# Kernel optimization log

Measured on AMD Instinct MI355X. Metric: run time of the kernel, lower is better.

Reference implementation:

```python
import jax, jax.numpy as jnp
import numpy as np

# ---- static config (LCNN wirenet) ----
K = 128            # fixed junction count per type (n_dyn_junc // n_type)
N_PTS0 = 32
N_PTS1 = 8
SCALE = N_PTS0 // N_PTS1   # maxpool1d kernel/stride = 4
DIM_LOI = 128
DIM_FC = 1024
FEATURE_DIM = 8
USE_COOD = 0.0
USE_SLOP = 0.0
HW = 128
B = 2
# static u<v pair indices (torch: meshgrid -> c = u < v), P = K*(K-1)/2
IU_np, IV_np = np.triu_indices(K, k=1)
P = IU_np.shape[0]
IU = jnp.asarray(IU_np, jnp.int32)
IV = jnp.asarray(IV_np, jnp.int32)
LAMBDA = jnp.linspace(0.0, 1.0, N_PTS0)[:, None]  # [32,1]


def setup_inputs() -> dict:
    key = jax.random.key(0)
    ks = jax.random.split(key, 8)
    inputs = jax.random.normal(ks[0], (B, 5, HW, HW), jnp.float32)
    features = jax.random.normal(ks[1], (B, 256, HW, HW), jnp.float32)
    fc1_w = jax.random.normal(ks[2], (DIM_LOI, 256), jnp.float32) * 0.05
    fc1_b = jnp.zeros((DIM_LOI,), jnp.float32)
    d_in = DIM_LOI * N_PTS1 + FEATURE_DIM  # 1032
    w1 = jax.random.normal(ks[3], (d_in, DIM_FC), jnp.float32) * 0.03
    b1 = jnp.zeros((DIM_FC,), jnp.float32)
    w2 = jax.random.normal(ks[4], (DIM_FC, DIM_FC), jnp.float32) * 0.03
    b2 = jnp.zeros((DIM_FC,), jnp.float32)
    w3 = jax.random.normal(ks[5], (DIM_FC, 1), jnp.float32) * 0.03
    b3 = jnp.zeros((1,), jnp.float32)
    return dict(inputs=inputs, features=features, fc1_w=fc1_w, fc1_b=fc1_b,
                w1=w1, b1=b1, w2=w2, b2=b2, w3=w3, b3=b3)


def _nms(a):
    # a: [1,H,W]; 3x3 max-pool NMS, keep only local maxima
    ap = jax.lax.reduce_window(a, -jnp.inf, jax.lax.max, (1, 3, 3), (1, 1, 1), 'SAME')
    return a * (a == ap).astype(a.dtype)


def _sample_lines(jmap, joff):
    # jmap: [1,H,W], joff: [1,2,H,W]  (inference path: dummy junc/Lpos)
    n_type = 1
    jm = _nms(jmap).reshape(n_type, -1)            # [1, HW*HW]
    jo = joff.reshape(n_type, 2, -1)
    score, index = jax.lax.top_k(jm, K)            # [1,K]
    y = (index // HW).astype(jnp.float32) + jnp.take_along_axis(jo[:, 0], index, 1) + 0.5
    x = (index % HW).astype(jnp.float32) + jnp.take_along_axis(jo[:, 1], index, 1) + 0.5
    xy = jnp.stack([y, x], -1)                     # [1,K,2]
    # inference dummies: junc=zeros(1,2), jtyp=zeros(1), Lpos=zeros(2,2)
    junc = jnp.zeros((1, 2), jnp.float32)
    jtyp = jnp.zeros((1,), jnp.int32)
    dist = jnp.sum((xy[:, :, None, :] - junc) ** 2, -1)  # [1,K,1]
    cost = jnp.min(dist, -1)
    match = jnp.argmin(dist, -1).astype(jnp.int32)       # [1,K]
    Njunc = 1
    match = jnp.where(jtyp[match] != jnp.arange(n_type, dtype=jnp.int32)[:, None], Njunc, match)
    match = jnp.where(cost > 1.5 * 1.5, Njunc, match).reshape(-1)  # [K]
    up, vp = match[IU], match[IV]
    Lpos = jnp.zeros((2, 2), jnp.float32)
    label = Lpos[up, vp]                           # [P]
    xyf = xy.reshape(n_type * K, 2)
    xyu, xyv = xyf[IU], xyf[IV]                    # [P,2]
    u2v = xyu - xyv
    u2v = u2v / jnp.clip(jnp.sqrt(jnp.sum(u2v ** 2, -1, keepdims=True)), 1e-6)
    feat = jnp.concatenate([
        xyu / HW * USE_COOD, xyv / HW * USE_COOD, u2v * USE_SLOP,
        (IU[:, None] > K).astype(jnp.float32), (IV[:, None] > K).astype(jnp.float32)], 1)  # [P,8]
    line = jnp.stack([xyu, xyv], 1)                # [P,2,2]
    return line, label, feat


def _loi_pool(xfeat, line):
    # xfeat: [C,H,W], line: [P,2,2] -> [P,C,N_PTS1]
    p = line[:, 0:1, :] * LAMBDA + line[:, 1:2, :] * (1.0 - LAMBDA) - 0.5  # [P,32,2]
    p = p.reshape(-1, 2)
    px, py = p[:, 0], p[:, 1]
    px0 = jnp.clip(jnp.floor(px), 0, HW - 1)
    py0 = jnp.clip(jnp.floor(py), 0, HW - 1)
    px1 = jnp.clip(px0 + 1, 0, HW - 1)
    py1 = jnp.clip(py0 + 1, 0, HW - 1)
    px0l = px0.astype(jnp.int32); py0l = py0.astype(jnp.int32)
    px1l = px1.astype(jnp.int32); py1l = py1.astype(jnp.int32)
    xp = (xfeat[:, px0l, py0l] * (px1 - px) * (py1 - py)
          + xfeat[:, px1l, py0l] * (px - px0) * (py1 - py)
          + xfeat[:, px0l, py1l] * (px1 - px) * (py - py0)
          + xfeat[:, px1l, py1l] * (px - px0) * (py - py0))  # [C, P*32]
    xp = xp.reshape(DIM_LOI, -1, N_PTS0).transpose(1, 0, 2)  # [P,C,32]
    # MaxPool1d(kernel=4, stride=4)
    return xp.reshape(xp.shape[0], DIM_LOI, N_PTS1, SCALE).max(-1)  # [P,C,8]


def _forward(inputs, features, fc1_w, fc1_b, w1, b1, w2, b2, w3, b3):
    b, _, r, c = inputs.shape
    out = jnp.transpose(inputs, (1, 0, 2, 3))       # [5,B,H,W]
    jmap_logits = out[0:2].reshape(1, 2, b, r, c)
    joff_logits = out[3:5].reshape(1, 2, b, r, c)
    jmap = jax.nn.softmax(jnp.transpose(jmap_logits, (2, 0, 1, 3, 4)), axis=2)[:, :, 1]  # [B,1,H,W]
    joff = jax.nn.sigmoid(jnp.transpose(joff_logits, (2, 0, 1, 3, 4))) - 0.5             # [B,1,2,H,W]
    # fc1: 1x1 conv 256 -> dim_loi
    xf = jnp.einsum('bchw,dc->bdhw', features, fc1_w) + fc1_b[None, :, None, None]
    lines, labels, feats = jax.vmap(_sample_lines)(jmap, joff)   # [B,P,2,2],[B,P],[B,P,8]
    # sample_lines runs under torch.no_grad()
    lines = jax.lax.stop_gradient(lines)
    labels = jax.lax.stop_gradient(labels)
    feats = jax.lax.stop_gradient(feats)
    xp = jax.vmap(_loi_pool)(xf, lines)             # [B,P,C,8]
    xv = xp.reshape(-1, N_PTS1 * DIM_LOI)           # [B*P, 1024] (C-major then pts)
    xv = jnp.concatenate([xv, feats.reshape(-1, FEATURE_DIM)], 1)  # [B*P, 1032]
    h = jax.nn.relu(xv @ w1 + b1)
    h = jax.nn.relu(h @ w2 + b2)
    scores = (h @ w3 + b3).reshape(-1)              # [B*P]
    return scores, labels.reshape(-1), lines


def reference(inputs, features, fc1_w, fc1_b, w1, b1, w2, b2, w3, b3):
    return _forward(inputs, features, fc1_w, fc1_b, w1, b1, w2, b2, w3, b3)
```

## Files before the change

### kernel.cpp

```cpp
#include <hip/hip_runtime.h>
#include <hip/hip_bf16.h>
#include <math.h>

#define HW 128
#define NPIX 16384
#define KTOP 128
#define PPAIR 8128
#define NB 2
#define DIMLOI 128
#define NROWS (NB*PPAIR)
#define MPAD 16384

typedef __bf16 bf16x8 __attribute__((ext_vector_type(8)));
typedef float floatx4 __attribute__((ext_vector_type(4)));
typedef float floatx8 __attribute__((ext_vector_type(8)));

__device__ __forceinline__ unsigned long long mk_key(float v, int idx) {
    return ((unsigned long long)__float_as_uint(v) << 32) |
           (unsigned long long)(0xFFFFFFFFu - (unsigned)idx);
}

__device__ __forceinline__ unsigned long long shfl_xor_u64(unsigned long long x, int m) {
    unsigned lo = (unsigned)x, hi = (unsigned)(x >> 32);
    lo = __shfl_xor(lo, m);
    hi = __shfl_xor(hi, m);
    return ((unsigned long long)hi << 32) | lo;
}

__device__ __forceinline__ void bitonic_stage(unsigned long long V[4], int lane, int j, int k) {
    if (j >= 64) {
        int qm = j >> 6;
        #pragma unroll
        for (int q = 0; q < 4; q++) {
            int p = q ^ qm;
            if (p > q) {
                int i = q * 64 + lane;
                bool desc = ((i & k) == 0);
                unsigned long long a = V[q], b = V[p];
                unsigned long long hi = a > b ? a : b, lo = a > b ? b : a;
                V[q] = desc ? hi : lo;
                V[p] = desc ? lo : hi;
            }
        }
    } else {
        #pragma unroll
        for (int q = 0; q < 4; q++) {
            int i = q * 64 + lane;
            unsigned long long p = shfl_xor_u64(V[q], j);
            bool lower = (lane & j) == 0;
            bool desc = ((i & k) == 0);
            bool keepmax = (desc == lower);
            unsigned long long mx = V[q] > p ? V[q] : p;
            unsigned long long mn = V[q] > p ? p : V[q];
            V[q] = keepmax ? mx : mn;
        }
    }
}

__device__ __forceinline__ void sort256_desc(unsigned long long V[4], int lane) {
    #pragma unroll
    for (int k = 2; k <= 256; k <<= 1)
        #pragma unroll
        for (int j = k >> 1; j >= 1; j >>= 1)
            bitonic_stage(V, lane, j, k);
}

__device__ __forceinline__ void merge256_desc(unsigned long long V[4], int lane) {
    #pragma unroll
    for (int j = 128; j >= 1; j >>= 1)
        bitonic_stage(V, lane, j, 256);
}

__global__ __launch_bounds__(256) void nms_sort_kernel(const float* __restrict__ inp,
                                                       unsigned long long* __restrict__ tkeys) {
    __shared__ float jm[10 * HW];
    __shared__ unsigned long long cand[256];
    __shared__ int scnt;
    int blk = blockIdx.x;
    int b   = blockIdx.y;
    int tid = threadIdx.x, lane = tid & 63;
    int r0  = blk * 8;
    int rlo = (r0 > 0) ? r0 - 1 : 0;
    int rhi = (r0 + 8 < HW) ? r0 + 8 : HW - 1;
    int nrows = rhi - rlo + 1;

    for (int i = tid; i < nrows * HW; i += 256) {
        int pix = rlo * HW + i;
        float l0 = inp[((long)b * 5 + 0) * NPIX + pix];
        float l1 = inp[((long)b * 5 + 1) * NPIX + pix];
        float m = fmaxf(l0, l1);
        float e0 = expf(l0 - m), e1 = expf(l1 - m);
        jm[i] = e1 / (e0 + e1);
    }
    cand[tid] = 0ull;
    if (tid == 0) scnt = 0;
    __syncthreads();

    #pragma unroll
    for (int i = 0; i < 4; i++) {
        int pl = i * 256 + tid;
        int r = r0 + (pl >> 7), c = pl & 127;
        float v = jm[(r - rlo) * HW + c];
        float m = v;
        for (int dr = -1; dr <= 1; dr++) {
            int rr = r + dr;
            if (rr < 0 || rr >= HW) continue;
            for (int dc = -1; dc <= 1; dc++) {
                int cc = c + dc;
                if (cc < 0 || cc >= HW) continue;
                m = fmaxf(m, jm[(rr - rlo) * HW + cc]);
            }
        }
        float nv = (v == m) ? v : 0.f;
        bool has = (nv > 0.f);
        unsigned long long mask = __ballot(has);
        int n = __popcll(mask);
        int wbase = 0;
        if (lane == 0 && n) wbase = atomicAdd(&scnt, n);
        wbase = __shfl(wbase, 0);
        if (has) {
            int pos = wbase + __popcll(mask & ((1ull << lane) - 1ull));
            if (pos < 256) cand[pos] = mk_key(nv, r * HW + c);
        }
    }
    __syncthreads();
    if (blk == 0 && tid < 128 && tid >= scnt) cand[tid] = mk_key(0.f, tid);
    __syncthreads();

    if (tid < 64) {
        unsigned long long V[4];
        #pragma unroll
        for (int q = 0; q < 4; q++) V[q] = cand[q * 64 + lane];
        sort256_desc(V, lane);
        #pragma unroll
        for (int q = 0; q < 2; q++)
            tkeys[((long)b * 16 + blk) * 128 + q * 64 + lane] = V[q];
    }
}

__global__ __launch_bounds__(512) void topk_merge_kernel(const unsigned long long* __restrict__ tkeys,
                                                         const float* __restrict__ inp,
                                                         float* __restrict__ xy) {
    __shared__ unsigned long long Lb[16 * 128];
    __shared__ unsigned long long Mb[8 * 128];
    int b = blockIdx.x;
    int tid = threadIdx.x, w = tid >> 6, lane = tid & 63;
    for (int i = tid; i < 16 * 128; i += 512) Lb[i] = tkeys[(long)b * 2048 + i];
    __syncthreads();

    unsigned long long* src = Lb;
    unsigned long long* dst = Mb;
    for (int nact = 8; nact >= 1; nact >>= 1) {
        unsigned long long V[4];
        if (w < nact) {
            #pragma unroll
            for (int q = 0; q < 2; q++) V[q] = src[(2 * w) * 128 + q * 64 + lane];
            #pragma unroll
            for (int q = 2; q < 4; q++) {
                int t = (q - 2) * 64 + lane;
                V[q] = src[(2 * w + 1) * 128 + 127 - t];
            }
            merge256_desc(V, lane);
        }
        __syncthreads();
        if (w < nact) {
            #pragma unroll
            for (int q = 0; q < 2; q++) dst[w * 128 + q * 64 + lane] = V[q];
        }
        __syncthreads();
        unsigned long long* tmp = src; src = dst; dst = tmp;
    }

    if (tid < KTOP) {
        unsigned long long key = src[tid];
        int wi = (int)(0xFFFFFFFFu - (unsigned)(key & 0xFFFFFFFFull));
        int row = wi >> 7, col = wi & 127;
        float l3 = inp[((long)b * 5 + 3) * NPIX + wi];
        float l4 = inp[((long)b * 5 + 4) * NPIX + wi];
        float joy = 1.f / (1.f + expf(-l3)) - 0.5f;
        float jox = 1.f / (1.f + expf(-l4)) - 0.5f;
        xy[(b * KTOP + tid) * 2 + 0] = (float)row + joy + 0.5f;
        xy[(b * KTOP + tid) * 2 + 1] = (float)col + jox + 0.5f;
    }
}

__device__ __forceinline__ void pair_uv(int p, int& u, int& v) {
    int uu = (int)((255.0 - sqrt(65025.0 - 8.0 * (double)p)) * 0.5);
    if (uu < 0) uu = 0;
    while (uu * (255 - uu) / 2 > p) uu--;
    while ((uu + 1) * (255 - (uu + 1)) / 2 <= p) uu++;
    u = uu;
    v = uu + 1 + (p - uu * (255 - uu) / 2);
}

__global__ void prep_weights(const float* __restrict__ w1, const float* __restrict__ w2,
                             const float* __restrict__ fc1w,
                             __hip_bfloat16* __restrict__ w1t, __hip_bfloat16* __restrict__ w2t,
                             __hip_bfloat16* __restrict__ fc1wb) {
    int z = blockIdx.z;
    int tx = threadIdx.x & 31, ty = threadIdx.x >> 5;
    if (z < 2) {
        const float* W = z ? w2 : w1;
        __hip_bfloat16* Wt = z ? w2t : w1t;
        __shared__ float t[32][33];
        int k0 = blockIdx.x * 32, n0 = blockIdx.y * 32;
        #pragma unroll
        for (int i = 0; i < 32; i += 8)
            t[ty + i][tx] = W[(long)(k0 + ty + i) * 1024 + n0 + tx];
        __syncthreads();
        #pragma unroll
        for (int i = 0; i < 32; i += 8)
            Wt[(long)(n0 + ty + i) * 1024 + k0 + tx] = __float2bfloat16(t[tx][ty + i]);
    } else {
        if (blockIdx.x < 4 && blockIdx.y < 8) {
            int r0 = blockIdx.x * 32, c0 = blockIdx.y * 32;
            #pragma unroll
            for (int i = 0; i < 32; i += 8) {
                long idx = (long)(r0 + ty + i) * 256 + c0 + tx;
                fc1wb[idx] = __float2bfloat16(fc1w[idx]);
            }
        }
    }
}

__device__ __forceinline__ void gload_lds16(const void* g, void* l) {
    __builtin_amdgcn_global_load_lds(
        (const __attribute__((address_space(1))) void*)g,
        (__attribute__((address_space(3))) void*)l, 16, 0, 0);
}

#define SA 264

__global__ __launch_bounds__(256) void xf_fused_kernel(
    const float* __restrict__ features, const __hip_bfloat16* __restrict__ fc1wb,
    const float* __restrict__ bias, __hip_bfloat16* __restrict__ C0) {
    __shared__ __align__(16) __bf16 A_lds[128 * SA];
    __shared__ __align__(16) unsigned short B_lds[128 * 32 * 8];
    int tid = threadIdx.x;
    int lane = tid & 63, wid = tid >> 6;
    int wr = wid >> 1, wc = wid & 1;
    int b = blockIdx.z;
    long pix0 = (long)blockIdx.x * 128;

    #pragma unroll
    for (int it = 0; it < 16; it++) {
        int slot = it * 256 + tid;
        int r = slot >> 5, s = slot & 31;
        int ss = s ^ (r & 7);
        gload_lds16(fc1wb + (size_t)r * 256 + ss * 8,
                    (char*)B_lds + (size_t)(it * 4096 + wid * 1024));
    }
    {
        int c = tid;
        const float* src = features + ((long)b * 256 + c) * NPIX + pix0;
        #pragma unroll
        for (int p4 = 0; p4 < 32; p4++) {
            floatx4 v = *(const floatx4*)(src + p4 * 4);
            #pragma unroll
            for (int e = 0; e < 4; e++)
                A_lds[(p4 * 4 + e) * SA + c] = (__bf16)v[e];
        }
    }
    __syncthreads();

    floatx4 acc[4][4];
    #pragma unroll
    for (int i = 0; i < 4; i++)
        #pragma unroll
        for (int j = 0; j < 4; j++) acc[i][j] = (floatx4){0.f, 0.f, 0.f, 0.f};

    int r15 = lane & 15;
    #pragma unroll
    for (int ks = 0; ks < 8; ks++) {
        int s = (lane >> 4) + ks * 4;
        bf16x8 af[4], bfr[4];
        #pragma unroll
        for (int mi = 0; mi < 4; mi++) {
            int R = wr * 64 + mi * 16 + r15;
            af[mi] = *(const bf16x8*)&A_lds[R * SA + s * 8];
        }
        #pragma unroll
        for (int ni = 0; ni < 4; ni++) {
            int Rn = wc * 64 + ni * 16 + r15;
            bfr[ni] = *(const bf16x8*)&B_lds[(size_t)Rn * 256 + ((s ^ (Rn & 7)) << 3)];
        }
        #pragma unroll
        for (int mi = 0; mi < 4; mi++)
            #pragma unroll
            for (int ni = 0; ni < 4; ni++)
                acc[mi][ni] = __builtin_amdgcn_mfma_f32_16x16x32_bf16(
                    af[mi], bfr[ni], acc[mi][ni], 0, 0, 0);
    }

    __hip_bfloat16* C = C0 + (long)b * NPIX * DIMLOI;
    #pragma unroll
    for (int ni = 0; ni < 4; ni++) {
        long c = wc * 64 + ni * 16 + r15;
        float bv = bias[c];
        #pragma unroll
        for (int mi = 0; mi < 4; mi++) {
            long rbase = pix0 + wr * 64 + mi * 16 + (lane >> 4) * 4;
            #pragma unroll
            for (int q = 0; q < 4; q++)
                C[(rbase + q) * (long)DIMLOI + c] = __float2bfloat16(acc[mi][ni][q] + bv);
        }
    }
}

#define BM 128
#define BN 128
#define BKK 64

template <bool SCORE>
__global__ __launch_bounds__(256) void gemm_mfma(
    const __hip_bfloat16* __restrict__ A, const __hip_bfloat16* __restrict__ Bt,
    const float* __restrict__ bias, __hip_bfloat16* __restrict__ C,
    int M, int N, int Kd,
    const float* __restrict__ w3, float* __restrict__ slab) {
    int bid = blockIdx.x;
    int xcd = bid & 7, j = bid >> 3;
    int mtpx = (M / BM) >> 3;
    int mt = xcd * mtpx + (j >> 3);
    int nt = j & 7;
    long row0 = (long)mt * BM, col0 = (long)nt * BN;

    __shared__ __align__(16) unsigned short LDSbuf[2 * BM * BKK];
    unsigned short* As = LDSbuf;
    unsigned short* Bs = LDSbuf + BM * BKK;
    int tid = threadIdx.x;
    int lane = tid & 63, wid = tid >> 6;
    int wr = wid >> 1, wc = wid & 1;

    floatx4 acc[4][4];
    #pragma unroll
    for (int i = 0; i < 4; i++)
        #pragma unroll
        for (int jj = 0; jj < 4; jj++) acc[i][jj] = (floatx4){0.f, 0.f, 0.f, 0.f};

    for (int k0 = 0; k0 < Kd; k0 += BKK) {
        #pragma unroll
        for (int it = 0; it < 4; it++) {
            int slot = wid * 256 + it * 64 + lane;
            int r = slot >> 3, s = slot & 7;
            int ss = s ^ (r & 7);
            gload_lds16(A + (row0 + r) * Kd + k0 + ss * 8,
                        (char*)As + (size_t)(wid * 4096 + it * 1024));
        }
        #pragma unroll
        for (int it = 0; it < 4; it++) {
            int slot = wid * 256 + it * 64 + lane;
            int r = slot >> 3, s = slot & 7;
            int ss = s ^ (r & 7);
            gload_lds16(Bt + (col0 + r) * Kd + k0 + ss * 8,
                        (char*)Bs + (size_t)(wid * 4096 + it * 1024));
        }
        __syncthreads();
        #pragma unroll
        for (int ks = 0; ks < 2; ks++) {
            bf16x8 af[4], bfr[4];
            int s = (lane >> 4) + ks * 4;
            #pragma unroll
            for (int mi = 0; mi < 4; mi++) {
                int R = wr * 64 + mi * 16 + (lane & 15);
                af[mi] = *(const bf16x8*)&As[R * BKK + ((s ^ (R & 7)) << 3)];
            }
            #pragma unroll
            for (int ni = 0; ni < 4; ni++) {
                int Rn = wc * 64 + ni * 16 + (lane & 15);
                bfr[ni] = *(const bf16x8*)&Bs[Rn * BKK + ((s ^ (Rn & 7)) << 3)];
            }
            #pragma unroll
            for (int mi = 0; mi < 4; mi++)
                #pragma unroll
                for (int ni = 0; ni < 4; ni++)
                    acc[mi][ni] = __builtin_amdgcn_mfma_f32_16x16x32_bf16(
                        af[mi], bfr[ni], acc[mi][ni], 0, 0, 0);
        }
        __syncthreads();
    }

    if constexpr (SCORE) {
        int ntile = (int)(col0 / BN);
        #pragma unroll
        for (int mi = 0; mi < 4; mi++) {
            #pragma unroll
            for (int q = 0; q < 4; q++) {
                float p = 0.f;
                #pragma unroll
                for (int ni = 0; ni < 4; ni++) {
                    long c = col0 + wc * 64 + ni * 16 + (lane & 15);
                    float v = fmaxf(acc[mi][ni][q] + bias[c], 0.f);
                    p += v * w3[c];
                }
                #pragma unroll
                for (int off = 1; off < 16; off <<= 1) p += __shfl_xor(p, off);
                if ((lane & 15) == 0) {
                    long row = row0 + wr * 64 + mi * 16 + (lane >> 4) * 4 + q;
                    slab[(long)(ntile * 2 + wc) * MPAD + row] = p;
                }
            }
        }
    } else {
        __hip_bfloat16* stg = (__hip_bfloat16*)LDSbuf + wid * 4096;
        #pragma unroll
        for (int ni = 0; ni < 4; ni++) {
            float bv = bias[col0 + wc * 64 + ni * 16 + (lane & 15)];
            #pragma unroll
            for (int mi = 0; mi < 4; mi++) {
                int rl = mi * 16 + (lane >> 4) * 4;
                #pragma unroll
                for (int q = 0; q < 4; q++) {
                    float v = fmaxf(acc[mi][ni][q] + bv, 0.f);
                    stg[(rl + q) * 64 + ni * 16 + (lane & 15)] = __float2bfloat16(v);
                }
            }
        }
        #pragma unroll
        for (int i = 0; i < 8; i++) {
            int rl = i * 8 + (lane >> 3), ch = lane & 7;
            bf16x8 v = *(const bf16x8*)&stg[rl * 64 + ch * 8];
            *(bf16x8*)&C[(row0 + wr * 64 + rl) * (long)N + col0 + wc * 64 + ch * 8] = v;
        }
    }
}

__global__ void score_reduce_kernel(const float* __restrict__ slab, const float* __restrict__ b3,
                                    float* __restrict__ out) {
    int r = blockIdx.x * 256 + threadIdx.x;
    if (r >= NROWS) return;
    float s = b3[0];
    #pragma unroll
    for (int i = 0; i < 16; i++) s += slab[(long)i * MPAD + r];
    out[r] = s;
}

__global__ __launch_bounds__(256) void loi_sample_kernel(
    const __hip_bfloat16* __restrict__ xf, const float* __restrict__ xy,
    __hip_bfloat16* __restrict__ xp, float* __restrict__ outp) {
    __shared__ int md[16 * 32 * 8];
    int tid = threadIdx.x;
    int bid = blockIdx.x;
    int swz = (bid & 7) * 128 + (bid >> 3);
    int rbase = swz * 16;

    {
        int pt0 = tid * 2;
        int sub = pt0 >> 5;
        int r = rbase + sub;
        int rm = (r < NROWS) ? r : NROWS - 1;
        int b = rm / PPAIR, p = rm % PPAIR;
        int u, v; pair_uv(p, u, v);
        float yu = xy[(b * KTOP + u) * 2 + 0], xu = xy[(b * KTOP + u) * 2 + 1];
        float yv = xy[(b * KTOP + v) * 2 + 0], xv = xy[(b * KTOP + v) * 2 + 1];
        if (((pt0 & 31) == 0) && r < NROWS) {
            float* lines = outp + 2 * NROWS;
            long base = (long)r * 4;
            lines[base + 0] = yu; lines[base + 1] = xu;
            lines[base + 2] = yv; lines[base + 3] = xv;
            outp[NROWS + r] = 0.f;
        }
        #pragma unroll
        for (int pp = 0; pp < 2; pp++) {
            int t = (pt0 + pp) & 31;
            float lam = (float)t * (1.0f / 31.0f);
            float px = yu * lam + yv * (1.f - lam) - 0.5f;
            float py = xu * lam + xv * (1.f - lam) - 0.5f;
            float px0 = fminf(fmaxf(floorf(px), 0.f), 127.f);
            float py0 = fminf(fmaxf(floorf(py), 0.f), 127.f);
            float px1 = fminf(px0 + 1.f, 127.f);
            float py1 = fminf(py0 + 1.f, 127.f);
            int ix0 = (int)px0, iy0 = (int)py0, ix1 = (int)px1, iy1 = (int)py1;
            int base = (pt0 + pp) * 8;
            md[base + 0] = (ix0 * HW + iy0) * (DIMLOI * 2);
            md[base + 1] = (ix1 * HW + iy0) * (DIMLOI * 2);
            md[base + 2] = (ix0 * HW + iy1) * (DIMLOI * 2);
            md[base + 3] = (ix1 * HW + iy1) * (DIMLOI * 2);
            md[base + 4] = __float_as_int((px1 - px) * (py1 - py));
            md[base + 5] = __float_as_int((px - px0) * (py1 - py));
            md[base + 6] = __float_as_int((px1 - px) * (py - py0));
            md[base + 7] = __float_as_int((px - px0) * (py - py0));
        }
    }
    __syncthreads();

    int sub2 = tid >> 4, o = tid & 15;
    int r = rbase + sub2;
    int rm = (r < NROWS) ? r : NROWS - 1;
    int b = rm / PPAIR;
    const char* xfb = (const char*)(xf + (long)b * NPIX * DIMLOI) + o * 16;
    floatx8 mx[8];
    #pragma unroll
    for (int q = 0; q < 8; q++)
        #pragma unroll
        for (int e = 0; e < 8; e++) mx[q][e] = -INFINITY;
    #pragma unroll
    for (int tt = 0; tt < 32; tt++) {
        const int* m = &md[(sub2 * 32 + tt) * 8];
        bf16x8 v00 = *(const bf16x8*)(xfb + m[0]);
        bf16x8 v10 = *(const bf16x8*)(xfb + m[1]);
        bf16x8 v01 = *(const bf16x8*)(xfb + m[2]);
        bf16x8 v11 = *(const bf16x8*)(xfb + m[3]);
        float w00 = __int_as_float(m[4]), w10 = __int_as_float(m[5]);
        float w01 = __int_as_float(m[6]), w11 = __int_as_float(m[7]);
        floatx8 s;
        #pragma unroll
        for (int e = 0; e < 8; e++)
            s[e] = (float)v00[e] * w00 + (float)v10[e] * w10 +
                   (float)v01[e] * w01 + (float)v11[e] * w11;
        mx[tt >> 2] = __builtin_elementwise_max(mx[tt >> 2], s);
    }
    __hip_bfloat16* rowp = xp + (long)r * 1024 + o * 64;
    #pragma unroll
    for (int e = 0; e < 8; e++) {
        bf16x8 outv;
        #pragma unroll
        for (int q = 0; q < 8; q++) outv[q] = (__bf16)mx[q][e];
        *(bf16x8*)(rowp + e * 8) = outv;
    }
}

extern "C" void kernel_launch(void* const* d_in, const int* in_sizes, int n_in,
                              void* d_out, int out_size, void* d_ws, size_t ws_size,
                              hipStream_t stream) {
    const float* inputs   = (const float*)d_in[0];
    const float* features = (const float*)d_in[1];
    const float* fc1_w    = (const float*)d_in[2];
    const float* fc1_b    = (const float*)d_in[3];
    const float* w1       = (const float*)d_in[4];
    const float* b1       = (const float*)d_in[5];
    const float* w2       = (const float*)d_in[6];
    const float* b2       = (const float*)d_in[7];
    const float* w3       = (const float*)d_in[8];
    const float* b3       = (const float*)d_in[9];
    float* out = (float*)d_out;
    float* ws  = (float*)d_ws;

    float* xy   = ws + 65536;
    __hip_bfloat16* xfb16 = (__hip_bfloat16*)(ws + 66048);
    __hip_bfloat16* xp    = (__hip_bfloat16*)(ws + 4260352);
    __hip_bfloat16* h1    = (__hip_bfloat16*)(ws + 12648960);
    float* slab           = ws + 21037568;
    __hip_bfloat16* w1t   = (__hip_bfloat16*)(ws + 21299712);
    __hip_bfloat16* w2t   = (__hip_bfloat16*)(ws + 21824000);
    __hip_bfloat16* fc1wb = (__hip_bfloat16*)(ws + 22348288);
    unsigned long long* tkeys = (unsigned long long*)(ws + 22364672);

    prep_weights<<<dim3(32, 32, 3), 256, 0, stream>>>(w1, w2, fc1_w, w1t, w2t, fc1wb);

    nms_sort_kernel<<<dim3(16, NB), 256, 0, stream>>>(inputs, tkeys);
    topk_merge_kernel<<<NB, 512, 0, stream>>>(tkeys, inputs, xy);

    xf_fused_kernel<<<dim3(NPIX / 128, 1, NB), 256, 0, stream>>>(
        features, fc1wb, fc1_b, xfb16);

    loi_sample_kernel<<<MPAD / 16, 256, 0, stream>>>(xfb16, xy, xp, out);

    gemm_mfma<false><<<(MPAD / BM) * 8, 256, 0, stream>>>(
        xp, w1t, b1, h1, MPAD, 1024, 1024, nullptr, nullptr);
    gemm_mfma<true><<<(MPAD / BM) * 8, 256, 0, stream>>>(
        h1, w2t, b2, nullptr, MPAD, 1024, 1024, w3, slab);
    score_reduce_kernel<<<(NROWS + 255) / 256, 256, 0, stream>>>(slab, b3, out);
}
```

Measured before the change: 167.8 us.

## Merge NMS-sort, fc1 projection and weight prep into one launch

Combines the NMS/sort kernel, the fc1 1x1-conv MFMA kernel and the weight transpose/bf16 kernel into one kernel that branches on block index. This removes two launches and lets the three independent jobs run at the same time on the GPU. Each fc1 block now converts fc1_w to bf16 itself and writes it into LDS, instead of loading a precomputed bf16 copy with global_load_lds. That repeats the conversion in every block. The fused kernel also reserves the largest LDS footprint for all block types, which may limit occupancy for the small NMS and transpose blocks. The fc1 branch launches 512 blocks, but those past the first 256 return immediately.

```diff
diff --git a/kernel.cpp b/kernel.cpp
--- a/kernel.cpp
+++ b/kernel.cpp
@@ -71,70 +71,196 @@
         bitonic_stage(V, lane, j, 256);
 }
 
-__global__ __launch_bounds__(256) void nms_sort_kernel(const float* __restrict__ inp,
-                                                       unsigned long long* __restrict__ tkeys) {
-    __shared__ float jm[10 * HW];
-    __shared__ unsigned long long cand[256];
-    __shared__ int scnt;
-    int blk = blockIdx.x;
-    int b   = blockIdx.y;
-    int tid = threadIdx.x, lane = tid & 63;
-    int r0  = blk * 8;
-    int rlo = (r0 > 0) ? r0 - 1 : 0;
-    int rhi = (r0 + 8 < HW) ? r0 + 8 : HW - 1;
-    int nrows = rhi - rlo + 1;
-
-    for (int i = tid; i < nrows * HW; i += 256) {
-        int pix = rlo * HW + i;
-        float l0 = inp[((long)b * 5 + 0) * NPIX + pix];
-        float l1 = inp[((long)b * 5 + 1) * NPIX + pix];
-        float m = fmaxf(l0, l1);
-        float e0 = expf(l0 - m), e1 = expf(l1 - m);
-        jm[i] = e1 / (e0 + e1);
-    }
-    cand[tid] = 0ull;
-    if (tid == 0) scnt = 0;
-    __syncthreads();
-
-    #pragma unroll
-    for (int i = 0; i < 4; i++) {
-        int pl = i * 256 + tid;
-        int r = r0 + (pl >> 7), c = pl & 127;
-        float v = jm[(r - rlo) * HW + c];
-        float m = v;
-        for (int dr = -1; dr <= 1; dr++) {
-            int rr = r + dr;
-            if (rr < 0 || rr >= HW) continue;
-            for (int dc = -1; dc <= 1; dc++) {
-                int cc = c + dc;
-                if (cc < 0 || cc >= HW) continue;
-                m = fmaxf(m, jm[(rr - rlo) * HW + cc]);
-            }
-        }
-        float nv = (v == m) ? v : 0.f;
-        bool has = (nv > 0.f);
-        unsigned long long mask = __ballot(has);
-        int n = __popcll(mask);
-        int wbase = 0;
-        if (lane == 0 && n) wbase = atomicAdd(&scnt, n);
-        wbase = __shfl(wbase, 0);
-        if (has) {
-            int pos = wbase + __popcll(mask & ((1ull << lane) - 1ull));
-            if (pos < 256) cand[pos] = mk_key(nv, r * HW + c);
-        }
-    }
-    __syncthreads();
-    if (blk == 0 && tid < 128 && tid >= scnt) cand[tid] = mk_key(0.f, tid);
-    __syncthreads();
-
-    if (tid < 64) {
-        unsigned long long V[4];
-        #pragma unroll
-        for (int q = 0; q < 4; q++) V[q] = cand[q * 64 + lane];
-        sort256_desc(V, lane);
-        #pragma unroll
-        for (int q = 0; q < 2; q++)
-            tkeys[((long)b * 16 + blk) * 128 + q * 64 + lane] = V[q];
+__device__ __forceinline__ void gload_lds16(const void* g, void* l) {
+    __builtin_amdgcn_global_load_lds(
+        (const __attribute__((address_space(1))) void*)g,
+        (__attribute__((address_space(3))) void*)l, 16, 0, 0);
+}
+
+__device__ __forceinline__ void pair_uv(int p, int& u, int& v) {
+    int uu = (int)((255.0 - sqrt(65025.0 - 8.0 * (double)p)) * 0.5);
+    if (uu < 0) uu = 0;
+    while (uu * (255 - uu) / 2 > p) uu--;
+    while ((uu + 1) * (255 - (uu + 1)) / 2 <= p) uu++;
+    u = uu;
+    v = uu + 1 + (p - uu * (255 - uu) / 2);
+}
+
+#define SA 264
+#define SMEM_BYTES (128 * SA * 2 + 128 * 256 * 2)
+
+__global__ __launch_bounds__(256) void mega_pre(
+    const float* __restrict__ inputs, const float* __restrict__ features,
+    const float* __restrict__ fc1_w, const float* __restrict__ fc1_b,
+    const float* __restrict__ w1, const float* __restrict__ w2,
+    __hip_bfloat16* __restrict__ w1t, __hip_bfloat16* __restrict__ w2t,
+    unsigned long long* __restrict__ tkeys, __hip_bfloat16* __restrict__ xfb16) {
+    __shared__ __align__(16) char smem[SMEM_BYTES];
+    int bid = blockIdx.x;
+    int tid = threadIdx.x;
+
+    if (bid < 32) {
+        float* jm = (float*)smem;
+        unsigned long long* cand = (unsigned long long*)(smem + 5120);
+        int* scnt = (int*)(smem + 7168);
+        int blk = bid & 15, b = bid >> 4;
+        int lane = tid & 63;
+        int r0  = blk * 8;
+        int rlo = (r0 > 0) ? r0 - 1 : 0;
+        int rhi = (r0 + 8 < HW) ? r0 + 8 : HW - 1;
+        int nrows = rhi - rlo + 1;
+
+        for (int i = tid; i < nrows * HW; i += 256) {
+            int pix = rlo * HW + i;
+            float l0 = inputs[((long)b * 5 + 0) * NPIX + pix];
+            float l1 = inputs[((long)b * 5 + 1) * NPIX + pix];
+            float m = fmaxf(l0, l1);
+            float e0 = expf(l0 - m), e1 = expf(l1 - m);
+            jm[i] = e1 / (e0 + e1);
+        }
+        cand[tid] = 0ull;
+        if (tid == 0) *scnt = 0;
+        __syncthreads();
+
+        #pragma unroll
+        for (int i = 0; i < 4; i++) {
+            int pl = i * 256 + tid;
+            int r = r0 + (pl >> 7), c = pl & 127;
+            float v = jm[(r - rlo) * HW + c];
+            float m = v;
+            for (int dr = -1; dr <= 1; dr++) {
+                int rr = r + dr;
+                if (rr < 0 || rr >= HW) continue;
+                for (int dc = -1; dc <= 1; dc++) {
+                    int cc = c + dc;
+                    if (cc < 0 || cc >= HW) continue;
+                    m = fmaxf(m, jm[(rr - rlo) * HW + cc]);
+                }
+            }
+            float nv = (v == m) ? v : 0.f;
+            bool has = (nv > 0.f);
+            unsigned long long mask = __ballot(has);
+            int n = __popcll(mask);
+            int wbase = 0;
+            if (lane == 0 && n) wbase = atomicAdd(scnt, n);
+            wbase = __shfl(wbase, 0);
+            if (has) {
+                int pos = wbase + __popcll(mask & ((1ull << lane) - 1ull));
+                if (pos < 256) cand[pos] = mk_key(nv, r * HW + c);
+            }
+        }
+        __syncthreads();
+        if (blk == 0 && tid < 128 && tid >= *scnt) cand[tid] = mk_key(0.f, tid);
+        __syncthreads();
+
+        if (tid < 64) {
+            unsigned long long V[4];
+            #pragma unroll
+            for (int q = 0; q < 4; q++) V[q] = cand[q * 64 + lane];
+            sort256_desc(V, lane);
+            #pragma unroll
+            for (int q = 0; q < 2; q++)
+                tkeys[((long)b * 16 + blk) * 128 + q * 64 + lane] = V[q];
+        }
+    } else if (bid < 544) {
+        __bf16* A_lds = (__bf16*)smem;
+        unsigned short* B_lds = (unsigned short*)(smem + 128 * SA * 2);
+        int i2 = bid - 32;
+        int b = i2 >> 8;
+        long pix0 = (long)(i2 & 255) * 64;
+        if (i2 >= 256) return;
+        b = i2 >> 7;
+        pix0 = (long)(i2 & 127) * 128;
+
+        int lane = tid & 63, wid = tid >> 6;
+        int wr = wid >> 1, wc = wid & 1;
+
+        {
+            int r = tid >> 1, ch = tid & 1;
+            const float* src = fc1_w + (size_t)r * 256 + ch * 128;
+            unsigned short* dstrow = B_lds + (size_t)r * 256;
+            int r7 = r & 7;
+            #pragma unroll
+            for (int q4 = 0; q4 < 32; q4++) {
+                floatx4 v = *(const floatx4*)(src + q4 * 4);
+                int c = ch * 128 + q4 * 4;
+                int addr = (((c >> 3) ^ r7) << 3) + (c & 7);
+                __hip_bfloat162* d0 = (__hip_bfloat162*)&dstrow[addr];
+                d0[0] = __hip_bfloat162{__float2bfloat16(v[0]), __float2bfloat16(v[1])};
+                d0[1] = __hip_bfloat162{__float2bfloat16(v[2]), __float2bfloat16(v[3])};
+            }
+        }
+        {
+            int c = tid;
+            const float* src = features + ((long)b * 256 + c) * NPIX + pix0;
+            #pragma unroll
+            for (int p4 = 0; p4 < 32; p4++) {
+                floatx4 v = *(const floatx4*)(src + p4 * 4);
+                #pragma unroll
+                for (int e = 0; e < 4; e++)
+                    A_lds[(p4 * 4 + e) * SA + c] = (__bf16)v[e];
+            }
+        }
+        __syncthreads();
+
+        floatx4 acc[4][4];
+        #pragma unroll
+        for (int i = 0; i < 4; i++)
+            #pragma unroll
+            for (int j = 0; j < 4; j++) acc[i][j] = (floatx4){0.f, 0.f, 0.f, 0.f};
+
+        int r15 = lane & 15;
+        #pragma unroll
+        for (int ks = 0; ks < 8; ks++) {
+            int s = (lane >> 4) + ks * 4;
+            bf16x8 af[4], bfr[4];
+            #pragma unroll
+            for (int mi = 0; mi < 4; mi++) {
+                int R = wr * 64 + mi * 16 + r15;
+                af[mi] = *(const bf16x8*)&A_lds[R * SA + s * 8];
+            }
+            #pragma unroll
+            for (int ni = 0; ni < 4; ni++) {
+                int Rn = wc * 64 + ni * 16 + r15;
+                bfr[ni] = *(const bf16x8*)&B_lds[(size_t)Rn * 256 + ((s ^ (Rn & 7)) << 3)];
+            }
+            #pragma unroll
+            for (int mi = 0; mi < 4; mi++)
+                #pragma unroll
+                for (int ni = 0; ni < 4; ni++)
+                    acc[mi][ni] = __builtin_amdgcn_mfma_f32_16x16x32_bf16(
+                        af[mi], bfr[ni], acc[mi][ni], 0, 0, 0);
+        }
+
+        __hip_bfloat16* C = xfb16 + (long)b * NPIX * DIMLOI;
+        #pragma unroll
+        for (int ni = 0; ni < 4; ni++) {
+            long c = wc * 64 + ni * 16 + r15;
+            float bv = fc1_b[c];
+            #pragma unroll
+            for (int mi = 0; mi < 4; mi++) {
+                long rbase = pix0 + wr * 64 + mi * 16 + (lane >> 4) * 4;
+                #pragma unroll
+                for (int q = 0; q < 4; q++)
+                    C[(rbase + q) * (long)DIMLOI + c] = __float2bfloat16(acc[mi][ni][q] + bv);
+            }
+        }
+    } else {
+        float (*t)[33] = (float(*)[33])smem;
+        int i3 = bid - 544;
+        int z = i3 >> 10;
+        int rem = i3 & 1023;
+        const float* W = z ? w2 : w1;
+        __hip_bfloat16* Wt = z ? w2t : w1t;
+        int k0 = (rem >> 5) * 32, n0 = (rem & 31) * 32;
+        int tx = tid & 31, ty = tid >> 5;
+        #pragma unroll
+        for (int i = 0; i < 32; i += 8)
+            t[ty + i][tx] = W[(long)(k0 + ty + i) * 1024 + n0 + tx];
+        __syncthreads();
+        #pragma unroll
+        for (int i = 0; i < 32; i += 8)
+            Wt[(long)(n0 + ty + i) * 1024 + k0 + tx] = __float2bfloat16(t[tx][ty + i]);
     }
 }
 
@@ -181,129 +307,6 @@
         float jox = 1.f / (1.f + expf(-l4)) - 0.5f;
         xy[(b * KTOP + tid) * 2 + 0] = (float)row + joy + 0.5f;
         xy[(b * KTOP + tid) * 2 + 1] = (float)col + jox + 0.5f;
-    }
-}
-
-__device__ __forceinline__ void pair_uv(int p, int& u, int& v) {
-    int uu = (int)((255.0 - sqrt(65025.0 - 8.0 * (double)p)) * 0.5);
-    if (uu < 0) uu = 0;
-    while (uu * (255 - uu) / 2 > p) uu--;
-    while ((uu + 1) * (255 - (uu + 1)) / 2 <= p) uu++;
-    u = uu;
-    v = uu + 1 + (p - uu * (255 - uu) / 2);
-}
-
-__global__ void prep_weights(const float* __restrict__ w1, const float* __restrict__ w2,
-                             const float* __restrict__ fc1w,
-                             __hip_bfloat16* __restrict__ w1t, __hip_bfloat16* __restrict__ w2t,
-                             __hip_bfloat16* __restrict__ fc1wb) {
-    int z = blockIdx.z;
-    int tx = threadIdx.x & 31, ty = threadIdx.x >> 5;
-    if (z < 2) {
-        const float* W = z ? w2 : w1;
-        __hip_bfloat16* Wt = z ? w2t : w1t;
-        __shared__ float t[32][33];
-        int k0 = blockIdx.x * 32, n0 = blockIdx.y * 32;
-        #pragma unroll
-        for (int i = 0; i < 32; i += 8)
-            t[ty + i][tx] = W[(long)(k0 + ty + i) * 1024 + n0 + tx];
-        __syncthreads();
-        #pragma unroll
-        for (int i = 0; i < 32; i += 8)
-            Wt[(long)(n0 + ty + i) * 1024 + k0 + tx] = __float2bfloat16(t[tx][ty + i]);
-    } else {
-        if (blockIdx.x < 4 && blockIdx.y < 8) {
-            int r0 = blockIdx.x * 32, c0 = blockIdx.y * 32;
-            #pragma unroll
-            for (int i = 0; i < 32; i += 8) {
-                long idx = (long)(r0 + ty + i) * 256 + c0 + tx;
-                fc1wb[idx] = __float2bfloat16(fc1w[idx]);
-            }
-        }
-    }
-}
-
-__device__ __forceinline__ void gload_lds16(const void* g, void* l) {
-    __builtin_amdgcn_global_load_lds(
-        (const __attribute__((address_space(1))) void*)g,
-        (__attribute__((address_space(3))) void*)l, 16, 0, 0);
-}
-
-#define SA 264
-
-__global__ __launch_bounds__(256) void xf_fused_kernel(
-    const float* __restrict__ features, const __hip_bfloat16* __restrict__ fc1wb,
-    const float* __restrict__ bias, __hip_bfloat16* __restrict__ C0) {
-    __shared__ __align__(16) __bf16 A_lds[128 * SA];
-    __shared__ __align__(16) unsigned short B_lds[128 * 32 * 8];
-    int tid = threadIdx.x;
-    int lane = tid & 63, wid = tid >> 6;
-    int wr = wid >> 1, wc = wid & 1;
-    int b = blockIdx.z;
-    long pix0 = (long)blockIdx.x * 128;
-
-    #pragma unroll
-    for (int it = 0; it < 16; it++) {
-        int slot = it * 256 + tid;
-        int r = slot >> 5, s = slot & 31;
-        int ss = s ^ (r & 7);
-        gload_lds16(fc1wb + (size_t)r * 256 + ss * 8,
-                    (char*)B_lds + (size_t)(it * 4096 + wid * 1024));
-    }
-    {
-        int c = tid;
-        const float* src = features + ((long)b * 256 + c) * NPIX + pix0;
-        #pragma unroll
-        for (int p4 = 0; p4 < 32; p4++) {
-            floatx4 v = *(const floatx4*)(src + p4 * 4);
-            #pragma unroll
-            for (int e = 0; e < 4; e++)
-                A_lds[(p4 * 4 + e) * SA + c] = (__bf16)v[e];
-        }
-    }
-    __syncthreads();
-
-    floatx4 acc[4][4];
-    #pragma unroll
-    for (int i = 0; i < 4; i++)
-        #pragma unroll
-        for (int j = 0; j < 4; j++) acc[i][j] = (floatx4){0.f, 0.f, 0.f, 0.f};
-
-    int r15 = lane & 15;
-    #pragma unroll
-    for (int ks = 0; ks < 8; ks++) {
-        int s = (lane >> 4) + ks * 4;
-        bf16x8 af[4], bfr[4];
-        #pragma unroll
-        for (int mi = 0; mi < 4; mi++) {
-            int R = wr * 64 + mi * 16 + r15;
-            af[mi] = *(const bf16x8*)&A_lds[R * SA + s * 8];
-        }
-        #pragma unroll
-        for (int ni = 0; ni < 4; ni++) {
-            int Rn = wc * 64 + ni * 16 + r15;
-            bfr[ni] = *(const bf16x8*)&B_lds[(size_t)Rn * 256 + ((s ^ (Rn & 7)) << 3)];
-        }
-        #pragma unroll
-        for (int mi = 0; mi < 4; mi++)
-            #pragma unroll
-            for (int ni = 0; ni < 4; ni++)
-                acc[mi][ni] = __builtin_amdgcn_mfma_f32_16x16x32_bf16(
-                    af[mi], bfr[ni], acc[mi][ni], 0, 0, 0);
-    }
-
-    __hip_bfloat16* C = C0 + (long)b * NPIX * DIMLOI;
-    #pragma unroll
-    for (int ni = 0; ni < 4; ni++) {
-        long c = wc * 64 + ni * 16 + r15;
-        float bv = bias[c];
-        #pragma unroll
-        for (int mi = 0; mi < 4; mi++) {
-            long rbase = pix0 + wr * 64 + mi * 16 + (lane >> 4) * 4;
-            #pragma unroll
-            for (int q = 0; q < 4; q++)
-                C[(rbase + q) * (long)DIMLOI + c] = __float2bfloat16(acc[mi][ni][q] + bv);
-        }
     }
 }
 
@@ -542,16 +545,12 @@
     float* slab           = ws + 21037568;
     __hip_bfloat16* w1t   = (__hip_bfloat16*)(ws + 21299712);
     __hip_bfloat16* w2t   = (__hip_bfloat16*)(ws + 21824000);
-    __hip_bfloat16* fc1wb = (__hip_bfloat16*)(ws + 22348288);
-    unsigned long long* tkeys = (unsigned long long*)(ws + 22364672);
-
-    prep_weights<<<dim3(32, 32, 3), 256, 0, stream>>>(w1, w2, fc1_w, w1t, w2t, fc1wb);
-
-    nms_sort_kernel<<<dim3(16, NB), 256, 0, stream>>>(inputs, tkeys);
+    unsigned long long* tkeys = (unsigned long long*)(ws + 22348288);
+
+    mega_pre<<<2592, 256, 0, stream>>>(inputs, features, fc1_w, fc1_b, w1, w2,
+                                       w1t, w2t, tkeys, xfb16);
+
     topk_merge_kernel<<<NB, 512, 0, stream>>>(tkeys, inputs, xy);
-
-    xf_fused_kernel<<<dim3(NPIX / 128, 1, NB), 256, 0, stream>>>(
-        features, fc1wb, fc1_b, xfb16);
 
     loi_sample_kernel<<<MPAD / 16, 256, 0, stream>>>(xfb16, xy, xp, out);
 
```

Result: faster. 161.9 us (-3.5%).
